# Kernel tuning notes

Measured on AMD Instinct MI355X. Metric: run time of the kernel, lower is better.

Reference implementation:

```python
import jax, jax.numpy as jnp
import numpy as np

B, H, S, D = 2, 12, 1024, 128
KQ, KK = 6, 11  # per-head conv kernel over (query, key) score plane


def setup_inputs() -> dict:
    key = jax.random.key(0)
    kq, kk, kv, kw = jax.random.split(key, 4)
    Q = jax.random.normal(kq, (B, H, S, D), dtype=jnp.float32)
    K = jax.random.normal(kk, (B, H, S, D), dtype=jnp.float32)
    V = jax.random.normal(kv, (B, H, S, D), dtype=jnp.float32)
    W = jax.random.normal(kw, (H, KQ, KK), dtype=jnp.float32) * 0.1
    return {"Q": Q, "K": K, "V": V, "W": W}


def reference(Q, K, V, W):
    # causal=True, softmax_scale = 1/sqrt(head_dim)  (module defaults)
    b, h, s, d = Q.shape
    _, kq, kk = W.shape
    pad_q = kq - 1            # causal padding along the query axis
    pad_k = (kk - 1) // 2     # 'same' padding along the key axis
    scale = 1.0 / np.sqrt(d).astype(np.float32)

    # Raw QK^T scores: [b, h, s_q, s_k]
    scores = jnp.einsum('bhqd,bhkd->bhqk', Q, K)

    # Causal: zero out future keys before the conv so the kernel cannot mix
    # in future information (matches the `causal` flag passed into the
    # fused qk_conv kernel; out-of-range tiles load as 0 in the Triton code).
    tril = jnp.tril(jnp.ones((s, s), dtype=bool))
    scores = jnp.where(tril[None, None], scores, 0.0)

    # Per-head 2D conv over the (q, k) plane: grouped conv with H groups,
    # kernel W[h] applied to head h's score map. Cross-correlation (PyTorch
    # conv semantics == lax.conv_general_dilated without kernel flip).
    conv = jax.lax.conv_general_dilated(
        scores,                      # [b, h, s, s] as NCHW
        W[:, None, :, :],            # [h, 1, kq, kk] as OIHW, groups=h
        window_strides=(1, 1),
        padding=((pad_q, 0), (pad_k, pad_k)),
        feature_group_count=h,
        dimension_numbers=('NCHW', 'OIHW', 'NCHW'),
    )

    # Scale, re-apply causal mask with the kernel's -1e6 fill, softmax, @V.
    logits = conv * scale + jnp.where(tril[None, None], 0.0, -1000000.0)
    P = jax.nn.softmax(logits, axis=-1)
    O = jnp.einsum('bhqk,bhkd->bhqd', P, V)
    return O
```

## Files before the change

### kernel.cpp

```cpp
#include <hip/hip_runtime.h>
#include <hip/hip_bf16.h>
#include <math.h>

#define B_ 2
#define H_ 12
#define S_ 1024
#define D_ 128
#define TQ 64
#define TK 32
#define SCALE 0.08838834764831843f

#define QROWS (S_ + 16)
#define KROWS (16 + S_ + 16)

#define QBLK 3120
#define KBLK 3168
#define VBLK 3072

typedef __attribute__((ext_vector_type(8))) short short8;
typedef __attribute__((ext_vector_type(4))) float floatx4;

__device__ __forceinline__ unsigned short f2b(float f) {
    return __builtin_bit_cast(unsigned short, __float2bfloat16(f));
}

__global__ __launch_bounds__(256) void prep_kernel(
    const float* __restrict__ Q, const float* __restrict__ K,
    const float* __restrict__ V,
    unsigned short* __restrict__ Qp, unsigned short* __restrict__ Kp,
    unsigned short* __restrict__ Vt)
{
    __shared__ float ls[32][33];
    const int bid = blockIdx.x;
    const int tid = threadIdx.x;
    if (bid < QBLK) {
        int e0 = (bid * 256 + tid) * 4;
        int bh = e0 / (QROWS * D_);
        int rem = e0 - bh * (QROWS * D_);
        int r = rem >> 7, d = rem & 127;
        int sr = r - 16;
        float4 v = make_float4(0.f, 0.f, 0.f, 0.f);
        if (sr >= 0 && sr < S_) v = *(const float4*)(Q + ((size_t)bh * S_ + sr) * D_ + d);
        ushort4 o; o.x = f2b(v.x); o.y = f2b(v.y); o.z = f2b(v.z); o.w = f2b(v.w);
        *(ushort4*)(Qp + ((size_t)bh * QROWS + r) * D_ + d) = o;
    } else if (bid < QBLK + KBLK) {
        int e0 = ((bid - QBLK) * 256 + tid) * 4;
        int bh = e0 / (KROWS * D_);
        int rem = e0 - bh * (KROWS * D_);
        int r = rem >> 7, d = rem & 127;
        int sr = r - 16;
        float4 v = make_float4(0.f, 0.f, 0.f, 0.f);
        if (sr >= 0 && sr < S_) v = *(const float4*)(K + ((size_t)bh * S_ + sr) * D_ + d);
        ushort4 o; o.x = f2b(v.x); o.y = f2b(v.y); o.z = f2b(v.z); o.w = f2b(v.w);
        *(ushort4*)(Kp + ((size_t)bh * KROWS + r) * D_ + d) = o;
    } else {
        int b = bid - (QBLK + KBLK);
        int dt = b & 3; int kt = (b >> 2) & 31; int bh = b >> 7;
        int lk = tid >> 3, ld = (tid & 7) * 4;
        float4 v = *(const float4*)(V + ((size_t)bh * S_ + kt * 32 + lk) * D_ + dt * 32 + ld);
        ls[lk][ld + 0] = v.x; ls[lk][ld + 1] = v.y; ls[lk][ld + 2] = v.z; ls[lk][ld + 3] = v.w;
        __syncthreads();
        int lk2 = tid >> 3, lc = (tid & 7) * 4;
        ushort4 o;
        o.x = f2b(ls[lc + 0][lk2]); o.y = f2b(ls[lc + 1][lk2]);
        o.z = f2b(ls[lc + 2][lk2]); o.w = f2b(ls[lc + 3][lk2]);
        *(ushort4*)(Vt + ((size_t)bh * D_ + dt * 32 + lk2) * S_ + kt * 32 + lc) = o;
    }
}

__global__ __launch_bounds__(256, 2) void conv_attn_mfma(
    const unsigned short* __restrict__ Qp,
    const unsigned short* __restrict__ Kp,
    const unsigned short* __restrict__ Vt,
    const float* __restrict__ W,
    float* __restrict__ O)
{
    __shared__ __align__(16) unsigned short Qs[80][136];
    __shared__ __align__(16) float sc[80][52];
    __shared__ __align__(16) unsigned short P[2][64][40];
    __shared__ __align__(16) float al_s[2][64];

    const int tid = threadIdx.x;
    const int wv = tid >> 6;
    const int ln = tid & 63;
    const int l15 = ln & 15;
    const int qd = ln >> 4;

    const int bid = blockIdx.x;
    const int bh = (bid & 7) * 3 + ((bid >> 3) % 3);
    const int qt = 15 - bid / 24;
    const int h = bh % H_;
    const int q0 = qt * TQ;

    const unsigned short* Qb = Qp + (size_t)bh * QROWS * D_;
    const unsigned short* Kb = Kp + (size_t)bh * KROWS * D_;
    const unsigned short* Vb = Vt + (size_t)bh * D_ * S_;
    const float* Wh = W + h * 66;

    for (int idx = tid; idx < 80 * 16; idx += 256) {
        int r = idx >> 4, c8 = (idx & 15) * 8;
        *(short8*)&Qs[r][c8] = *(const short8*)(Qb + (size_t)(q0 + r) * D_ + c8);
    }
    __syncthreads();

    int nt_t[4], mt_t[4], kro_t[4];
    #pragma unroll
    for (int t = 0; t < 4; ++t) {
        int u = wv * 4 + t;
        int nt = u / 5;
        nt_t[t] = nt; mt_t[t] = u - nt * 5;
        kro_t[t] = 8 + nt * 16 + l15;
    }

    const int p = 16 * wv + (ln >> 2);
    const int c0 = (ln & 3) * 8;

    floatx4 acc[4][2];
    #pragma unroll
    for (int mt = 0; mt < 4; ++mt)
        #pragma unroll
        for (int n2 = 0; n2 < 2; ++n2)
            acc[mt][n2] = (floatx4){0.f, 0.f, 0.f, 0.f};
    float m_run = -INFINITY, l_run = 0.f;

    const int nkt = 2 * qt + 2;
    for (int kt = 0; kt < nkt; ++kt) {
        const int k0 = kt * TK;
        const int par = kt & 1;

        #pragma unroll
        for (int t = 0; t < 4; ++t) {
            if (wv * 4 + t < 15) {
                const int nt = nt_t[t], mt = mt_t[t];
                const unsigned short* krow = Kb + (size_t)(k0 + kro_t[t]) * D_;
                short8 kf[4], qf[4];
                #pragma unroll
                for (int kc = 0; kc < 4; ++kc) {
                    kf[kc] = *(const short8*)(krow + kc * 32 + qd * 8);
                    qf[kc] = *(const short8*)&Qs[mt * 16 + l15][kc * 32 + qd * 8];
                }
                floatx4 s = {0.f, 0.f, 0.f, 0.f};
                #pragma unroll
                for (int kc = 0; kc < 4; ++kc)
                    s = __builtin_amdgcn_mfma_f32_16x16x32_bf16(qf[kc], kf[kc], s, 0, 0, 0);
                const int qrow = q0 - 16 + mt * 16 + qd * 4;
                const int kcol = k0 - 8 + nt * 16 + l15;
                #pragma unroll
                for (int reg = 0; reg < 4; ++reg)
                    sc[mt * 16 + qd * 4 + reg][nt * 16 + l15] =
                        (kcol <= qrow + reg) ? s[reg] : 0.f;
            }
        }
        __syncthreads();

        float pl[8];
        #pragma unroll
        for (int jj = 0; jj < 8; ++jj) pl[jj] = 0.f;
        #pragma unroll
        for (int i = 0; i < 6; ++i) {
            const float* rp = &sc[p + 11 + i][c0];
            float4 b0 = ((const float4*)rp)[0];
            float4 b1 = ((const float4*)rp)[1];
            float4 b2 = ((const float4*)rp)[2];
            float4 b3 = ((const float4*)rp)[3];
            float4 b4 = ((const float4*)rp)[4];
            float4 b5 = ((const float4*)rp)[5];
            float win[24] = {b0.x, b0.y, b0.z, b0.w, b1.x, b1.y, b1.z, b1.w,
                             b2.x, b2.y, b2.z, b2.w, b3.x, b3.y, b3.z, b3.w,
                             b4.x, b4.y, b4.z, b4.w, b5.x, b5.y, b5.z, b5.w};
            #pragma unroll
            for (int j = 0; j < 11; ++j) {
                const float w = Wh[i * 11 + j];
                #pragma unroll
                for (int jj = 0; jj < 8; ++jj)
                    pl[jj] = fmaf(w, win[3 + j + jj], pl[jj]);
            }
        }

        {
            const int q = q0 + p;
            float lg[8];
            float mx = -1e30f;
            #pragma unroll
            for (int jj = 0; jj < 8; ++jj) {
                const int k = k0 + c0 + jj;
                lg[jj] = (k <= q) ? pl[jj] * SCALE : -1e30f;
                mx = fmaxf(mx, lg[jj]);
            }
            mx = fmaxf(mx, __shfl_xor(mx, 1));
            mx = fmaxf(mx, __shfl_xor(mx, 2));
            const float nm = fmaxf(m_run, mx);
            const float alpha = __expf(m_run - nm);
            float sum = 0.f;
            short8 pb;
            #pragma unroll
            for (int jj = 0; jj < 8; ++jj) {
                float pv = __expf(lg[jj] - nm);
                sum += pv;
                pb[jj] = (short)f2b(pv);
            }
            sum += __shfl_xor(sum, 1);
            sum += __shfl_xor(sum, 2);
            l_run = l_run * alpha + sum;
            m_run = nm;
            *(short8*)&P[par][p][c0] = pb;
            if ((ln & 3) == 0) al_s[par][p] = alpha;
        }
        __syncthreads();

        {
            float4 al4[4];
            #pragma unroll
            for (int mt = 0; mt < 4; ++mt)
                al4[mt] = *(const float4*)&al_s[par][mt * 16 + qd * 4];
            #pragma unroll
            for (int mt = 0; mt < 4; ++mt) {
                #pragma unroll
                for (int n2 = 0; n2 < 2; ++n2) {
                    acc[mt][n2][0] *= al4[mt].x;
                    acc[mt][n2][1] *= al4[mt].y;
                    acc[mt][n2][2] *= al4[mt].z;
                    acc[mt][n2][3] *= al4[mt].w;
                }
            }
            short8 pf[4];
            #pragma unroll
            for (int mt = 0; mt < 4; ++mt)
                pf[mt] = *(const short8*)&P[par][mt * 16 + l15][qd * 8];
            short8 vfr[2];
            #pragma unroll
            for (int n2 = 0; n2 < 2; ++n2) {
                const int d = (2 * wv + n2) * 16 + l15;
                vfr[n2] = *(const short8*)(Vb + (size_t)d * S_ + k0 + qd * 8);
            }
            #pragma unroll
            for (int n2 = 0; n2 < 2; ++n2)
                #pragma unroll
                for (int mt = 0; mt < 4; ++mt)
                    acc[mt][n2] = __builtin_amdgcn_mfma_f32_16x16x32_bf16(pf[mt], vfr[n2], acc[mt][n2], 0, 0, 0);
        }
    }

    __syncthreads();
    if ((ln & 3) == 0) al_s[0][p] = 1.0f / l_run;
    __syncthreads();
    {
        float4 inv4[4];
        #pragma unroll
        for (int mt = 0; mt < 4; ++mt)
            inv4[mt] = *(const float4*)&al_s[0][mt * 16 + qd * 4];
        float* Ob = O + (size_t)bh * S_ * D_;
        #pragma unroll
        for (int mt = 0; mt < 4; ++mt) {
            const float iv[4] = {inv4[mt].x, inv4[mt].y, inv4[mt].z, inv4[mt].w};
            #pragma unroll
            for (int reg = 0; reg < 4; ++reg) {
                const int row = mt * 16 + qd * 4 + reg;
                #pragma unroll
                for (int n2 = 0; n2 < 2; ++n2) {
                    const int col = (2 * wv + n2) * 16 + l15;
                    Ob[(size_t)(q0 + row) * D_ + col] = acc[mt][n2][reg] * iv[reg];
                }
            }
        }
    }
}

extern "C" void kernel_launch(void* const* d_in, const int* in_sizes, int n_in,
                              void* d_out, int out_size, void* d_ws, size_t ws_size,
                              hipStream_t stream) {
    const float* Q = (const float*)d_in[0];
    const float* K = (const float*)d_in[1];
    const float* V = (const float*)d_in[2];
    const float* W = (const float*)d_in[3];
    float* O = (float*)d_out;

    unsigned short* Qp = (unsigned short*)d_ws;
    unsigned short* Kp = (unsigned short*)((char*)d_ws + 6389760);
    unsigned short* Vt = (unsigned short*)((char*)d_ws + 12877824);

    prep_kernel<<<dim3(QBLK + KBLK + VBLK), dim3(256), 0, stream>>>(Q, K, V, Qp, Kp, Vt);
    conv_attn_mfma<<<dim3(B_ * H_ * (S_ / TQ)), dim3(256), 0, stream>>>(Qp, Kp, Vt, W, O);
}
```

Baseline: 233.6 us.

## Compute score-plane conv with MFMA and give each wave its own query rows

```diff
diff --git a/kernel.cpp b/kernel.cpp
--- a/kernel.cpp
+++ b/kernel.cpp
@@ -16,6 +16,8 @@
 #define QBLK 3120
 #define KBLK 3168
 #define VBLK 3072
+
+#define SCW 56
 
 typedef __attribute__((ext_vector_type(8))) short short8;
 typedef __attribute__((ext_vector_type(4))) float floatx4;
@@ -76,9 +78,9 @@
     float* __restrict__ O)
 {
     __shared__ __align__(16) unsigned short Qs[80][136];
-    __shared__ __align__(16) float sc[80][52];
-    __shared__ __align__(16) unsigned short P[2][64][40];
-    __shared__ __align__(16) float al_s[2][64];
+    __shared__ __align__(16) unsigned short sc[2][80][SCW];
+    __shared__ __align__(16) unsigned short Pst[4][16][40];
+    __shared__ float Wf[66];
 
     const int tid = threadIdx.x;
     const int wv = tid >> 6;
@@ -88,14 +90,16 @@
 
     const int bid = blockIdx.x;
     const int bh = (bid & 7) * 3 + ((bid >> 3) % 3);
-    const int qt = 15 - bid / 24;
+    const int g = bid / 24;
+    const int qt = (g & 1) ? (g >> 1) : (15 - (g >> 1));
     const int h = bh % H_;
     const int q0 = qt * TQ;
 
     const unsigned short* Qb = Qp + (size_t)bh * QROWS * D_;
     const unsigned short* Kb = Kp + (size_t)bh * KROWS * D_;
     const unsigned short* Vb = Vt + (size_t)bh * D_ * S_;
-    const float* Wh = W + h * 66;
+
+    if (tid < 66) Wf[tid] = W[h * 66 + tid];
 
     for (int idx = tid; idx < 80 * 16; idx += 256) {
         int r = idx >> 4, c8 = (idx & 15) * 8;
@@ -103,165 +107,134 @@
     }
     __syncthreads();
 
-    int nt_t[4], mt_t[4], kro_t[4];
+    short8 bfr[6];
+    #pragma unroll
+    for (int i = 0; i < 6; ++i) {
+        short8 b;
+        #pragma unroll
+        for (int j = 0; j < 8; ++j) {
+            int widx = qd * 8 + j - l15 - 3;
+            float v = (widx >= 0 && widx <= 10) ? Wf[i * 11 + widx] : 0.f;
+            b[j] = (short)f2b(v);
+        }
+        bfr[i] = b;
+    }
+
+    const int nu = (wv == 3) ? 3 : 4;
+    int nt_t[4], mt_t[4];
     #pragma unroll
     for (int t = 0; t < 4; ++t) {
         int u = wv * 4 + t;
-        int nt = u / 5;
-        nt_t[t] = nt; mt_t[t] = u - nt * 5;
-        kro_t[t] = 8 + nt * 16 + l15;
-    }
-
-    const int p = 16 * wv + (ln >> 2);
-    const int c0 = (ln & 3) * 8;
-
-    floatx4 acc[4][2];
+        if (u > 14) u = 14;
+        nt_t[t] = u / 5; mt_t[t] = u - (u / 5) * 5;
+    }
+
+    floatx4 acc[8];
     #pragma unroll
-    for (int mt = 0; mt < 4; ++mt)
-        #pragma unroll
-        for (int n2 = 0; n2 < 2; ++n2)
-            acc[mt][n2] = (floatx4){0.f, 0.f, 0.f, 0.f};
-    float m_run = -INFINITY, l_run = 0.f;
+    for (int nt = 0; nt < 8; ++nt) acc[nt] = (floatx4){0.f, 0.f, 0.f, 0.f};
+    float m_run[4] = {-INFINITY, -INFINITY, -INFINITY, -INFINITY};
+    float l_run[4] = {0.f, 0.f, 0.f, 0.f};
 
     const int nkt = 2 * qt + 2;
     for (int kt = 0; kt < nkt; ++kt) {
         const int k0 = kt * TK;
-        const int par = kt & 1;
-
-        #pragma unroll
-        for (int t = 0; t < 4; ++t) {
-            if (wv * 4 + t < 15) {
-                const int nt = nt_t[t], mt = mt_t[t];
-                const unsigned short* krow = Kb + (size_t)(k0 + kro_t[t]) * D_;
-                short8 kf[4], qf[4];
-                #pragma unroll
-                for (int kc = 0; kc < 4; ++kc) {
-                    kf[kc] = *(const short8*)(krow + kc * 32 + qd * 8);
-                    qf[kc] = *(const short8*)&Qs[mt * 16 + l15][kc * 32 + qd * 8];
-                }
-                floatx4 s = {0.f, 0.f, 0.f, 0.f};
-                #pragma unroll
-                for (int kc = 0; kc < 4; ++kc)
-                    s = __builtin_amdgcn_mfma_f32_16x16x32_bf16(qf[kc], kf[kc], s, 0, 0, 0);
-                const int qrow = q0 - 16 + mt * 16 + qd * 4;
-                const int kcol = k0 - 8 + nt * 16 + l15;
-                #pragma unroll
-                for (int reg = 0; reg < 4; ++reg)
-                    sc[mt * 16 + qd * 4 + reg][nt * 16 + l15] =
-                        (kcol <= qrow + reg) ? s[reg] : 0.f;
-            }
+        const int buf = kt & 1;
+
+        for (int t = 0; t < nu; ++t) {
+            const int nt = nt_t[t], mt = mt_t[t];
+            const unsigned short* krow = Kb + (size_t)(k0 + 8 + nt * 16 + l15) * D_;
+            floatx4 s = {0.f, 0.f, 0.f, 0.f};
+            #pragma unroll
+            for (int kc = 0; kc < 4; ++kc) {
+                short8 kf = *(const short8*)(krow + kc * 32 + qd * 8);
+                short8 qf = *(const short8*)&Qs[mt * 16 + l15][kc * 32 + qd * 8];
+                s = __builtin_amdgcn_mfma_f32_16x16x32_bf16(qf, kf, s, 0, 0, 0);
+            }
+            const int qrow = q0 - 16 + mt * 16 + qd * 4;
+            const int kcol = k0 - 8 + nt * 16 + l15;
+            #pragma unroll
+            for (int reg = 0; reg < 4; ++reg)
+                sc[buf][mt * 16 + qd * 4 + reg][nt * 16 + l15] =
+                    (kcol <= qrow + reg) ? f2b(s[reg]) : (unsigned short)0;
         }
         __syncthreads();
 
-        float pl[8];
-        #pragma unroll
-        for (int jj = 0; jj < 8; ++jj) pl[jj] = 0.f;
-        #pragma unroll
-        for (int i = 0; i < 6; ++i) {
-            const float* rp = &sc[p + 11 + i][c0];
-            float4 b0 = ((const float4*)rp)[0];
-            float4 b1 = ((const float4*)rp)[1];
-            float4 b2 = ((const float4*)rp)[2];
-            float4 b3 = ((const float4*)rp)[3];
-            float4 b4 = ((const float4*)rp)[4];
-            float4 b5 = ((const float4*)rp)[5];
-            float win[24] = {b0.x, b0.y, b0.z, b0.w, b1.x, b1.y, b1.z, b1.w,
-                             b2.x, b2.y, b2.z, b2.w, b3.x, b3.y, b3.z, b3.w,
-                             b4.x, b4.y, b4.z, b4.w, b5.x, b5.y, b5.z, b5.w};
-            #pragma unroll
-            for (int j = 0; j < 11; ++j) {
-                const float w = Wh[i * 11 + j];
-                #pragma unroll
-                for (int jj = 0; jj < 8; ++jj)
-                    pl[jj] = fmaf(w, win[3 + j + jj], pl[jj]);
-            }
-        }
-
-        {
-            const int q = q0 + p;
-            float lg[8];
-            float mx = -1e30f;
-            #pragma unroll
-            for (int jj = 0; jj < 8; ++jj) {
-                const int k = k0 + c0 + jj;
-                lg[jj] = (k <= q) ? pl[jj] * SCALE : -1e30f;
-                mx = fmaxf(mx, lg[jj]);
-            }
+        floatx4 cv[2];
+        #pragma unroll
+        for (int n = 0; n < 2; ++n) {
+            floatx4 c4 = {0.f, 0.f, 0.f, 0.f};
+            #pragma unroll
+            for (int i = 0; i < 6; ++i) {
+                short8 af = *(const short8*)&sc[buf][wv * 16 + l15 + 11 + i][n * 16 + qd * 8];
+                c4 = __builtin_amdgcn_mfma_f32_16x16x32_bf16(af, bfr[i], c4, 0, 0, 0);
+            }
+            cv[n] = c4;
+        }
+
+        float lg[2][4];
+        #pragma unroll
+        for (int n = 0; n < 2; ++n)
+            #pragma unroll
+            for (int reg = 0; reg < 4; ++reg) {
+                const int q = q0 + wv * 16 + qd * 4 + reg;
+                const int k = k0 + n * 16 + l15;
+                lg[n][reg] = (k <= q) ? cv[n][reg] * SCALE : -1e30f;
+            }
+        float alpha[4];
+        float p[2][4];
+        #pragma unroll
+        for (int reg = 0; reg < 4; ++reg) {
+            float mx = fmaxf(lg[0][reg], lg[1][reg]);
             mx = fmaxf(mx, __shfl_xor(mx, 1));
             mx = fmaxf(mx, __shfl_xor(mx, 2));
-            const float nm = fmaxf(m_run, mx);
-            const float alpha = __expf(m_run - nm);
-            float sum = 0.f;
-            short8 pb;
-            #pragma unroll
-            for (int jj = 0; jj < 8; ++jj) {
-                float pv = __expf(lg[jj] - nm);
-                sum += pv;
-                pb[jj] = (short)f2b(pv);
-            }
+            mx = fmaxf(mx, __shfl_xor(mx, 4));
+            mx = fmaxf(mx, __shfl_xor(mx, 8));
+            const float nm = fmaxf(m_run[reg], mx);
+            alpha[reg] = __expf(m_run[reg] - nm);
+            p[0][reg] = __expf(lg[0][reg] - nm);
+            p[1][reg] = __expf(lg[1][reg] - nm);
+            float sum = p[0][reg] + p[1][reg];
             sum += __shfl_xor(sum, 1);
             sum += __shfl_xor(sum, 2);
-            l_run = l_run * alpha + sum;
-            m_run = nm;
-            *(short8*)&P[par][p][c0] = pb;
-            if ((ln & 3) == 0) al_s[par][p] = alpha;
-        }
-        __syncthreads();
+            sum += __shfl_xor(sum, 4);
+            sum += __shfl_xor(sum, 8);
+            l_run[reg] = l_run[reg] * alpha[reg] + sum;
+            m_run[reg] = nm;
+        }
+
+        #pragma unroll
+        for (int n = 0; n < 2; ++n)
+            #pragma unroll
+            for (int reg = 0; reg < 4; ++reg)
+                Pst[wv][qd * 4 + reg][n * 16 + l15] = f2b(p[n][reg]);
+
+        #pragma unroll
+        for (int nt = 0; nt < 8; ++nt)
+            #pragma unroll
+            for (int reg = 0; reg < 4; ++reg)
+                acc[nt][reg] *= alpha[reg];
 
         {
-            float4 al4[4];
-            #pragma unroll
-            for (int mt = 0; mt < 4; ++mt)
-                al4[mt] = *(const float4*)&al_s[par][mt * 16 + qd * 4];
-            #pragma unroll
-            for (int mt = 0; mt < 4; ++mt) {
-                #pragma unroll
-                for (int n2 = 0; n2 < 2; ++n2) {
-                    acc[mt][n2][0] *= al4[mt].x;
-                    acc[mt][n2][1] *= al4[mt].y;
-                    acc[mt][n2][2] *= al4[mt].z;
-                    acc[mt][n2][3] *= al4[mt].w;
-                }
-            }
-            short8 pf[4];
-            #pragma unroll
-            for (int mt = 0; mt < 4; ++mt)
-                pf[mt] = *(const short8*)&P[par][mt * 16 + l15][qd * 8];
-            short8 vfr[2];
-            #pragma unroll
-            for (int n2 = 0; n2 < 2; ++n2) {
-                const int d = (2 * wv + n2) * 16 + l15;
-                vfr[n2] = *(const short8*)(Vb + (size_t)d * S_ + k0 + qd * 8);
-            }
-            #pragma unroll
-            for (int n2 = 0; n2 < 2; ++n2)
-                #pragma unroll
-                for (int mt = 0; mt < 4; ++mt)
-                    acc[mt][n2] = __builtin_amdgcn_mfma_f32_16x16x32_bf16(pf[mt], vfr[n2], acc[mt][n2], 0, 0, 0);
-        }
-    }
-
-    __syncthreads();
-    if ((ln & 3) == 0) al_s[0][p] = 1.0f / l_run;
-    __syncthreads();
+            short8 pf = *(const short8*)&Pst[wv][l15][qd * 8];
+            #pragma unroll
+            for (int nt = 0; nt < 8; ++nt) {
+                short8 vf = *(const short8*)(Vb + (size_t)(nt * 16 + l15) * S_ + k0 + qd * 8);
+                acc[nt] = __builtin_amdgcn_mfma_f32_16x16x32_bf16(pf, vf, acc[nt], 0, 0, 0);
+            }
+        }
+    }
+
     {
-        float4 inv4[4];
-        #pragma unroll
-        for (int mt = 0; mt < 4; ++mt)
-            inv4[mt] = *(const float4*)&al_s[0][mt * 16 + qd * 4];
+        float inv[4];
+        #pragma unroll
+        for (int reg = 0; reg < 4; ++reg) inv[reg] = 1.0f / l_run[reg];
         float* Ob = O + (size_t)bh * S_ * D_;
         #pragma unroll
-        for (int mt = 0; mt < 4; ++mt) {
-            const float iv[4] = {inv4[mt].x, inv4[mt].y, inv4[mt].z, inv4[mt].w};
-            #pragma unroll
-            for (int reg = 0; reg < 4; ++reg) {
-                const int row = mt * 16 + qd * 4 + reg;
-                #pragma unroll
-                for (int n2 = 0; n2 < 2; ++n2) {
-                    const int col = (2 * wv + n2) * 16 + l15;
-                    Ob[(size_t)(q0 + row) * D_ + col] = acc[mt][n2][reg] * iv[reg];
-                }
-            }
+        for (int reg = 0; reg < 4; ++reg) {
+            const int row = q0 + wv * 16 + qd * 4 + reg;
+            #pragma unroll
+            for (int nt = 0; nt < 8; ++nt)
+                Ob[(size_t)row * D_ + nt * 16 + l15] = acc[nt][reg] * inv[reg];
         }
     }
 }
```

Measured after the change: 244.6 us. 1.05x slower.
